# Performance work log

Hardware: AMD Instinct MI355X
Metric: run time of the kernel (lower is better)

The kernel has to match this reference:

```python
import jax, jax.numpy as jnp
import numpy as np

B_SZ = 8
G = 2048
D_MODEL = 512
D_STATE = 128
D_CONV = 4
EXPAND = 2
HEADDIM = 64
D_INNER = EXPAND * D_MODEL          # 1024
NHEADS = D_INNER // HEADDIM         # 16
CONV_DIM = D_INNER + 2 * D_STATE    # 1280
D_IN_PROJ = 2 * D_INNER + 2 * D_STATE + NHEADS  # 2320
ID_DIM = 128
CHR_DIM = 64
N_CHR = 25
F_LOCUS = 32
PATH_DIM = 128
GENE_FEAT = ID_DIM + PATH_DIM + 2 * CHR_DIM  # 384
N_PERT = 10000
P_DIM = 128


def silu(x):
    return x * jax.nn.sigmoid(x)


def causal_dw_conv(x, w, b):
    # x: (B,L,C), w: (C,K), b: (C,)  causal depthwise conv (left pad K-1)
    K = w.shape[1]
    L = x.shape[1]
    xp = jnp.pad(x, ((0, 0), (K - 1, 0), (0, 0)))
    out = b[None, None, :]
    for k in range(K):
        out = out + xp[:, k:k + L, :] * w[:, k][None, None, :]
    return out


def mamba2(u, in_w, conv_w, conv_b, dt_bias, A_log, Dp, norm_w, out_w):
    # u: (B,L,d_model) -> (B,L,d_model); mamba_ssm Mamba2 defaults, ngroups=1
    Bb, L, _ = u.shape
    zxbcdt = u @ in_w.T                                   # (B,L,D_IN_PROJ)
    z = zxbcdt[..., :D_INNER]
    xBC = zxbcdt[..., D_INNER:D_INNER + CONV_DIM]
    dt = zxbcdt[..., D_INNER + CONV_DIM:]                 # (B,L,H)
    xBC = silu(causal_dw_conv(xBC, conv_w, conv_b))
    x = xBC[..., :D_INNER].reshape(Bb, L, NHEADS, HEADDIM)
    Bm = xBC[..., D_INNER:D_INNER + D_STATE]              # (B,L,N)
    Cm = xBC[..., D_INNER + D_STATE:]                     # (B,L,N)
    dt = jax.nn.softplus(dt + dt_bias)                    # (B,L,H)
    dA = jnp.exp(dt * (-jnp.exp(A_log)))                  # (B,L,H)

    def step(h, inp):
        dA_t, dt_t, B_t, C_t, x_t = inp
        h = dA_t[:, :, None, None] * h + jnp.einsum('bh,bn,bhp->bhpn', dt_t, B_t, x_t)
        y = jnp.einsum('bhpn,bn->bhp', h, C_t)
        return h, y

    h0 = jnp.zeros((Bb, NHEADS, HEADDIM, D_STATE), u.dtype)
    xs = (dA.transpose(1, 0, 2), dt.transpose(1, 0, 2),
          Bm.transpose(1, 0, 2), Cm.transpose(1, 0, 2), x.transpose(1, 0, 2, 3))
    _, ys = jax.lax.scan(step, h0, xs)                    # ys: (L,B,H,P)
    y = ys.transpose(1, 0, 2, 3) + Dp[None, None, :, None] * x
    y = y.reshape(Bb, L, D_INNER)
    # gated RMSNorm (norm_before_gate=False): norm(y * silu(z))
    y = y * silu(z)
    y = y * jax.lax.rsqrt(jnp.mean(y * y, axis=-1, keepdims=True) + 1e-5) * norm_w
    return y @ out_w.T


def setup_inputs() -> dict:
    key = jax.random.key(0)
    ks = iter(jax.random.split(key, 48))

    def nrm(shape, scale):
        return jax.random.normal(next(ks), shape, jnp.float32) * scale

    inp = {}
    inp['perturbation_idx'] = jax.random.randint(next(ks), (B_SZ,), 0, N_PERT)
    inp['chr_idx'] = jax.random.randint(next(ks), (G,), 0, N_CHR)
    inp['locus_fourier'] = nrm((G, 2 * F_LOCUS), 1.0)
    inp['pathway_features'] = nrm((G, PATH_DIM), 1.0)
    inp['pert_emb'] = nrm((N_PERT, P_DIM), 0.02)
    inp['gene_id_emb'] = nrm((G, ID_DIM), 0.02)
    inp['chr_emb'] = nrm((N_CHR, CHR_DIM), 0.02)
    inp['locus_w'] = nrm((CHR_DIM, 2 * F_LOCUS), (2 * F_LOCUS) ** -0.5)
    inp['locus_b'] = jnp.zeros((CHR_DIM,), jnp.float32)
    inp['cond_w'] = nrm((GENE_FEAT, P_DIM), P_DIM ** -0.5)
    inp['cond_b'] = jnp.zeros((GENE_FEAT,), jnp.float32)
    inp['in_w'] = nrm((D_MODEL, GENE_FEAT), GENE_FEAT ** -0.5)
    inp['in_b'] = jnp.zeros((D_MODEL,), jnp.float32)
    inp['head_w'] = nrm((1, D_MODEL), D_MODEL ** -0.5)
    inp['head_b'] = jnp.zeros((1,), jnp.float32)
    for p in ('f_', 'b_'):
        inp[p + 'in_w'] = nrm((D_IN_PROJ, D_MODEL), D_MODEL ** -0.5)
        inp[p + 'conv_w'] = nrm((CONV_DIM, D_CONV), D_CONV ** -0.5)
        inp[p + 'conv_b'] = jnp.zeros((CONV_DIM,), jnp.float32)
        inp[p + 'dt_bias'] = nrm((NHEADS,), 0.5)
        inp[p + 'A_log'] = jnp.log(jax.random.uniform(next(ks), (NHEADS,), jnp.float32, 1.0, 16.0))
        inp[p + 'D'] = jnp.ones((NHEADS,), jnp.float32)
        inp[p + 'norm_w'] = jnp.ones((D_INNER,), jnp.float32)
        inp[p + 'out_w'] = nrm((D_MODEL, D_INNER), D_INNER ** -0.5)
    return inp


def reference(perturbation_idx, chr_idx, locus_fourier, pathway_features,
              pert_emb, gene_id_emb, chr_emb, locus_w, locus_b,
              cond_w, cond_b, in_w, in_b, head_w, head_b,
              f_in_w, f_conv_w, f_conv_b, f_dt_bias, f_A_log, f_D, f_norm_w, f_out_w,
              b_in_w, b_conv_w, b_conv_b, b_dt_bias, b_A_log, b_D, b_norm_w, b_out_w):
    B = perturbation_idx.shape[0]
    cond = pert_emb[perturbation_idx] @ cond_w.T + cond_b          # (B, GENE_FEAT)
    e_chr = chr_emb[chr_idx]                                        # (G, CHR_DIM)
    e_locus = jax.nn.gelu(locus_fourier @ locus_w.T + locus_b, approximate=False)
    gene_feat = jnp.concatenate([gene_id_emb, pathway_features, e_chr, e_locus], axis=1)  # (G, GENE_FEAT)
    seq = jnp.concatenate([cond[:, None, :],
                           jnp.broadcast_to(gene_feat[None], (B,) + gene_feat.shape)], axis=1)
    seq = seq @ in_w.T + in_b                                       # (B, G+1, d_model)
    h_fwd = mamba2(seq, f_in_w, f_conv_w, f_conv_b, f_dt_bias, f_A_log, f_D, f_norm_w, f_out_w)
    h_bwd = jnp.flip(mamba2(jnp.flip(seq, axis=1), b_in_w, b_conv_w, b_conv_b,
                            b_dt_bias, b_A_log, b_D, b_norm_w, b_out_w), axis=1)
    H = h_fwd + h_bwd
    return H[:, 1:, :] @ head_w.T + head_b                          # (B, G, 1)
```

## Files before the change

kernel.cpp:

```cpp
#include <hip/hip_runtime.h>
#include <hip/hip_bf16.h>
#include <hip/hip_fp16.h>
#include <math.h>

#define DPROJ 2320
#define CONVD 1280

typedef __attribute__((ext_vector_type(8))) short bf16x8;
typedef __attribute__((ext_vector_type(4))) float f32x4;

__device__ __forceinline__ float siluf(float x) { return x / (1.f + __expf(-x)); }
__device__ __forceinline__ float bfu(unsigned short s) { return __uint_as_float(((unsigned)s) << 16); }
__device__ __forceinline__ unsigned short f2bf(float f) {
    unsigned u = __float_as_uint(f);
    unsigned r = (u + 0x7FFFu + ((u >> 16) & 1u)) >> 16;
    return (unsigned short)r;
}
__device__ __forceinline__ unsigned short f2h(float f) {
    __half h = __float2half(f);
    return *(unsigned short*)&h;
}
__device__ __forceinline__ float h2f(unsigned short s) {
    __half h = *(__half*)&s;
    return __half2float(h);
// ... 165 lines not shown
#pragma unroll
        for (int kk = 0; kk < 16; ++kk) {
            float4 a = *(const float4*)&As[kk][ty * 4];
            float4 w = *(const float4*)&Ws[kk][tx * 4];
            float aa[4] = {a.x, a.y, a.z, a.w}, ww[4] = {w.x, w.y, w.z, w.w};
#pragma unroll
            for (int i = 0; i < 4; ++i)
#pragma unroll
                for (int j = 0; j < 4; ++j) acc[i][j] += aa[i] * ww[j];
        }
    }
#pragma unroll
    for (int i = 0; i < 4; ++i) {
        const int m = bm + ty * 4 + i;
        if (m >= M) continue;
#pragma unroll
        for (int j = 0; j < 4; ++j) {
            const int n = bn + tx * 4 + j;
            if (n >= N) continue;
            float v = acc[i][j] + (bias ? bias[n] : 0.f);
            if (act == 1) v = 0.5f * v * (1.f + erff(v * 0.70710678118654752f));
            C[(size_t)m * ldc + n] = v;
        }
    }
}


__global__ void elem_kernel(const float* __restrict__ zxf, const float* __restrict__ zxb,
                            const float* __restrict__ zxc,
                            const float* __restrict__ fDtB, const float* __restrict__ bDtB,
                            unsigned short* __restrict__ szF, unsigned short* __restrict__ szB,
                            float* __restrict__ dtFsT, float* __restrict__ dtBsT,
                            float* __restrict__ dtFp) {
    size_t idx = (size_t)blockIdx.x * 256 + threadIdx.x;
    const size_t SZ = 2048UL * 1024;
    if (idx < SZ) {
        size_t j = idx >> 10, d = idx & 1023;
        szF[idx] = f2h(siluf(zxf[j * DPROJ + d]));
    } else if (idx < 2 * SZ) {
        size_t k = idx - SZ;
        size_t j = k >> 10, d = k & 1023;
        szB[k] = f2h(siluf(zxb[j * DPROJ + d]));
    } else if (idx < 2 * SZ + 32768) {
        int k = (int)(idx - 2 * SZ);
        int r = k >> 4, hh = k & 15;
        float raw = zxf[(size_t)r * DPROJ + 2304 + hh] + fDtB[hh];
        dtFsT[hh * 2048 + r] = (raw > 20.f) ? raw : log1pf(expf(raw));
    } else if (idx < 2 * SZ + 65536) {
        int k = (int)(idx - 2 * SZ - 32768);
        int r = k >> 4, hh = k & 15;
        float raw = zxb[(size_t)(2047 - r) * DPROJ + 2304 + hh] + bDtB[hh];
        dtBsT[hh * 2048 + r] = (raw > 20.f) ? raw : log1pf(expf(raw));
    } else if (idx < 2 * SZ + 65536 + 128) {
        int k = (int)(idx - 2 * SZ - 65536);
        int b = k >> 4, hh = k & 15;
        float raw = zxc[(size_t)b * DPROJ + 2304 + hh] + fDtB[hh];
        dtFp[k] = (raw > 20.f) ? raw : log1pf(expf(raw));
    }
}

__global__ void cum_kernel(const float* __restrict__ dtFsT, const float* __restrict__ dtBsT,
                           const float* __restrict__ fAlog, const float* __restrict__ bAlog,
                           float* __restrict__ cumF, float* __restrict__ cumB) {
    int id = blockIdx.x * 256 + threadIdx.x;
    int dir = id >> 9, k = id & 511, h = k >> 5, c = k & 31;
    const float* dtT = dir ? dtBsT : dtFsT;
    const float* Al = dir ? bAlog : fAlog;
    float* cum = dir ? cumB : cumF;
    float a = -expf(Al[h]);
    float acc = 0.f;
    for (int s4 = 0; s4 < 16; ++s4) {
        float4 v = *(const float4*)&dtT[h * 2048 + c * 64 + s4 * 4];
        float4 o;
        acc += v.x * a; o.x = acc;
        acc += v.y * a; o.y = acc;
        acc += v.z * a; o.z = acc;
        acc += v.w * a; o.w = acc;
        *(float4*)&cum[h * 2048 + c * 64 + s4 * 4] = o;
    }
}


__global__ void convFsh_kernel(const float* __restrict__ zxf, const float* __restrict__ cw,
                               const float* __restrict__ cb, float* __restrict__ outp,
                               unsigned short* __restrict__ bc16, unsigned short* __restrict__ x16) {
    int idx = blockIdx.x * 256 + threadIdx.x;
    if (idx >= 2045 * 1280) return;
    int t4 = idx / 1280, c = idx % 1280;
    float4 w4 = *(const float4*)&cw[c * 4];
    float acc = cb[c];
    acc += zxf[(size_t)(t4 + 0) * DPROJ + 1024 + c] * w4.x;
    acc += zxf[(size_t)(t4 + 1) * DPROJ + 1024 + c] * w4.y;
    acc += zxf[(size_t)(t4 + 2) * DPROJ + 1024 + c] * w4.z;
    acc += zxf[(size_t)(t4 + 3) * DPROJ + 1024 + c] * w4.w;
    float r = siluf(acc);
    outp[idx] = r;
    if (c >= 1024) bc16[(size_t)t4 * 256 + (c - 1024)] = f2bf(r);
    else           x16[(size_t)t4 * 1024 + c] = f2h(r);
}

__global__ void convFpb_kernel(const float* __restrict__ zxf, const float* __restrict__ zxc,
                               const float* __restrict__ cw, const float* __restrict__ cb,
                               float* __restrict__ outp, unsigned short* __restrict__ bc16,
                               unsigned short* __restrict__ x16) {
    int idx = blockIdx.x * 256 + threadIdx.x;
    int b = idx / 5120;
    int r = idx % 5120;
    int t = r / 1280, c = r % 1280;
    float4 w4 = *(const float4*)&cw[c * 4];
    float w[4] = {w4.x, w4.y, w4.z, w4.w};
    float acc = cb[c];
#pragma unroll
    for (int k = 0; k < 4; ++k) {
        int j = t - 3 + k;
        float x = 0.f;
        if (j == 0)      x = zxc[(size_t)b * DPROJ + 1024 + c];
        else if (j >= 1) x = zxf[(size_t)(j - 1) * DPROJ + 1024 + c];
        acc += x * w[k];
    }
    float rr = siluf(acc);
    outp[idx] = rr;
    if (c >= 1024) bc16[(size_t)(b * 4 + t) * 256 + (c - 1024)] = f2bf(rr);
    else           x16[(size_t)(b * 4 + t) * 1024 + c] = f2h(rr);
}

__global__ void convBsh_kernel(const float* __restrict__ zxb, const float* __restrict__ cw,
                               const float* __restrict__ cb, float* __restrict__ outp,
                               unsigned short* __restrict__ bc16, unsigned short* __restrict__ x16) {
    int idx = blockIdx.x * 256 + threadIdx.x;
    int s = idx / 1280, c = idx % 1280;
    float4 w4 = *(const float4*)&cw[c * 4];
    float w[4] = {w4.x, w4.y, w4.z, w4.w};
    float acc = cb[c];
#pragma unroll
    for (int k = 0; k < 4; ++k) {
        int j = s - 3 + k;
        if (j >= 0) acc += zxb[(size_t)(2047 - j) * DPROJ + 1024 + c] * w[k];
    }
    float r = siluf(acc);
    outp[idx] = r;
    if (c >= 1024) bc16[(size_t)s * 256 + (c - 1024)] = f2bf(r);
    else           x16[(size_t)s * 1024 + c] = f2h(r);
}


__global__ __launch_bounds__(256) void intra_kernel(
    const unsigned short* __restrict__ bcF, const unsigned short* __restrict__ bcFp,
    const unsigned short* __restrict__ bcB,
    const float* __restrict__ convFs, const float* __restrict__ convFp,
    const float* __restrict__ convBs,
    const float* __restrict__ dtFsT, const float* __restrict__ dtBsT,
    const float* __restrict__ cumF, const float* __restrict__ cumB,
    unsigned short* __restrict__ YiF0, unsigned short* __restrict__ YiFs,
    unsigned short* __restrict__ YiB,
    unsigned short* __restrict__ UF0, unsigned short* __restrict__ UFs,
    unsigned short* __restrict__ UB) {
    __shared__ __align__(16) unsigned char smraw[63232];
    unsigned short* Bt = (unsigned short*)smraw;
    unsigned short* Ct = (unsigned short*)(smraw + 17408);
    unsigned short* Sm = (unsigned short*)(smraw + 17408);
    unsigned short* BT = (unsigned short*)(smraw + 34816);
    unsigned short* XT = (unsigned short*)(smraw + 53248);
    float* scum = (float*)(smraw + 62464);
    float* sdt  = scum + 64;
    float* se   = scum + 128;

    const int iid = blockIdx.x;
    int dir, b = 0, h, c;
    unsigned short *Yout, *Uout;
    if (iid < 128)      { dir = 0; b = iid >> 4; h = iid & 15; c = 0;
                          Yout = YiF0 + (size_t)(b * 16 + h) * 4096; Uout = UF0 + (size_t)(b * 16 + h) * 8192; }
    else if (iid < 624) { int k = iid - 128; dir = 0; c = 1 + (k >> 4); h = k & 15;
                          Yout = YiFs + (size_t)(c * 16 + h) * 4096; Uout = UFs + (size_t)(c * 16 + h) * 8192; }
    else                { int k = iid - 624; dir = 1; c = k >> 4; h = k & 15;
                          Yout = YiB + (size_t)(c * 16 + h) * 4096;  Uout = UB + (size_t)(c * 16 + h) * 8192; }
    const float* dtAT = dir ? dtBsT : dtFsT;
    const float* cumA = dir ? cumB : cumF;

    const int tid = threadIdx.x;
    const int lane = tid & 63, wave = tid >> 6;
    const int quad = lane >> 4, l15 = lane & 15;

    {
        int r = tid >> 2, q = tid & 3;
        const unsigned short* bsrc;
        const float* xrow;
        if (dir == 0) {
            int t = 64 * c + 1 + r;
            if (t < 4) { bsrc = bcFp + (size_t)(b * 4 + t) * 256; xrow = convFp + (size_t)(b * 4 + t) * CONVD; }
            else       { bsrc = bcF + (size_t)(t - 4) * 256;      xrow = convFs + (size_t)(t - 4) * CONVD; }
        } else {
            int s = 64 * c + r;
            bsrc = bcB + (size_t)s * 256;
            xrow = convBs + (size_t)s * CONVD;
        }
#pragma unroll
        for (int i = 0; i < 4; ++i) {
            int n0 = q * 32 + i * 8;
            uint4 v = *(const uint4*)&bsrc[n0];
            *(uint4*)&Bt[r * 136 + n0] = v;
            const unsigned short* pv = (const unsigned short*)&v;
#pragma unroll
            for (int jj = 0; jj < 8; ++jj) BT[(n0 + jj) * 72 + r] = pv[jj];
        }
#pragma unroll
        for (int i = 0; i < 4; ++i) {
            int n0 = q * 32 + i * 8;
            uint4 v = *(const uint4*)&bsrc[128 + n0];
            *(uint4*)&Ct[r * 136 + n0] = v;
        }
#pragma unroll
        for (int i = 0; i < 4; ++i) {
            int p0 = (q + 4 * i) * 4;
            float4 v = *(const float4*)&xrow[h * 64 + p0];
            XT[(p0 + 0) * 72 + r] = f2bf(v.x);
            XT[(p0 + 1) * 72 + r] = f2bf(v.y);
            XT[(p0 + 2) * 72 + r] = f2bf(v.z);
            XT[(p0 + 3) * 72 + r] = f2bf(v.w);
        }
        if (tid < 64) {
            int j = 64 * c + tid;
            scum[tid] = cumA[h * 2048 + j];
            sdt[tid] = dtAT[h * 2048 + j];
        }
    }
    __syncthreads();
    if (tid < 64) se[tid] = __expf(scum[63] - scum[tid]) * sdt[tid];

    const int tm = (wave >> 1) * 32, sn = (wave & 1) * 32;
    f32x4 acc1[2][2];
#pragma unroll
    for (int i = 0; i < 2; ++i)
#pragma unroll
        for (int j = 0; j < 2; ++j) acc1[i][j] = (f32x4){0.f, 0.f, 0.f, 0.f};
#pragma unroll
    for (int ks = 0; ks < 4; ++ks) {
        bf16x8 af[2], bfr[2];
#pragma unroll
        for (int i = 0; i < 2; ++i)
            af[i] = *(const bf16x8*)&Ct[(tm + i * 16 + l15) * 136 + ks * 32 + quad * 8];
#pragma unroll
        for (int j = 0; j < 2; ++j)
            bfr[j] = *(const bf16x8*)&Bt[(sn + j * 16 + l15) * 136 + ks * 32 + quad * 8];
#pragma unroll
        for (int i = 0; i < 2; ++i)
#pragma unroll
            for (int j = 0; j < 2; ++j)
                acc1[i][j] = __builtin_amdgcn_mfma_f32_16x16x32_bf16(af[i], bfr[j], acc1[i][j], 0, 0, 0);
    }
    __syncthreads();

#pragma unroll
    for (int j = 0; j < 2; ++j) {
        int s = sn + j * 16 + l15;
        float cs = scum[s], ds = sdt[s];
#pragma unroll
        for (int i = 0; i < 2; ++i) {
#pragma unroll
            for (int r = 0; r < 4; ++r) {
                int t = tm + i * 16 + quad * 4 + r;
                float v = (s <= t) ? __expf(scum[t] - cs) * ds * acc1[i][j][r] : 0.f;
                Sm[t * 72 + s] = f2bf(v);
            }
        }
    }
    __syncthreads();

    const int pm = (wave >> 1) * 32, tn = (wave & 1) * 32;
    f32x4 acc2[2][2];
#pragma unroll
    for (int i = 0; i < 2; ++i)
#pragma unroll
        for (int j = 0; j < 2; ++j) acc2[i][j] = (f32x4){0.f, 0.f, 0.f, 0.f};
#pragma unroll
    for (int ks = 0; ks < 2; ++ks) {
        bf16x8 af[2], bfr[2];
#pragma unroll
        for (int i = 0; i < 2; ++i)
            af[i] = *(const bf16x8*)&XT[(pm + i * 16 + l15) * 72 + ks * 32 + quad * 8];
#pragma unroll
        for (int j = 0; j < 2; ++j)
            bfr[j] = *(const bf16x8*)&Sm[(tn + j * 16 + l15) * 72 + ks * 32 + quad * 8];
#pragma unroll
        for (int i = 0; i < 2; ++i)
#pragma unroll
            for (int j = 0; j < 2; ++j)
                acc2[i][j] = __builtin_amdgcn_mfma_f32_16x16x32_bf16(af[i], bfr[j], acc2[i][j], 0, 0, 0);
    }
#pragma unroll
    for (int i = 0; i < 2; ++i)
#pragma unroll
        for (int j = 0; j < 2; ++j) {
            int t = tn + j * 16 + l15;
            int p0 = pm + i * 16 + quad * 4;
            ushort4 o = make_ushort4(f2bf(acc2[i][j][0]), f2bf(acc2[i][j][1]),
                                     f2bf(acc2[i][j][2]), f2bf(acc2[i][j][3]));
            *(ushort4*)&Yout[t * 64 + p0] = o;
        }

    const int nm = wave * 32;
    f32x4 acc3[2][4];
#pragma unroll
    for (int i = 0; i < 2; ++i)
#pragma unroll
        for (int j = 0; j < 4; ++j) acc3[i][j] = (f32x4){0.f, 0.f, 0.f, 0.f};
#pragma unroll
    for (int ks = 0; ks < 2; ++ks) {
        float ev[8];
#pragma unroll
        for (int jj = 0; jj < 8; ++jj) ev[jj] = se[ks * 32 + quad * 8 + jj];
        bf16x8 bfx[4];
#pragma unroll
        for (int j = 0; j < 4; ++j) {
            bf16x8 xs = *(const bf16x8*)&XT[(j * 16 + l15) * 72 + ks * 32 + quad * 8];
#pragma unroll
            for (int jj = 0; jj < 8; ++jj)
                bfx[j][jj] = (short)f2bf(bfu((unsigned short)xs[jj]) * ev[jj]);
        }
        bf16x8 af[2];
#pragma unroll
        for (int i = 0; i < 2; ++i)
            af[i] = *(const bf16x8*)&BT[(nm + i * 16 + l15) * 72 + ks * 32 + quad * 8];
#pragma unroll
        for (int i = 0; i < 2; ++i)
#pragma unroll
            for (int j = 0; j < 4; ++j)
                acc3[i][j] = __builtin_amdgcn_mfma_f32_16x16x32_bf16(af[i], bfx[j], acc3[i][j], 0, 0, 0);
    }
#pragma unroll
    for (int i = 0; i < 2; ++i)
#pragma unroll
        for (int j = 0; j < 4; ++j) {
            int p = j * 16 + l15;
            int n0 = nm + i * 16 + quad * 4;
            ushort4 o = make_ushort4(f2bf(acc3[i][j][0]), f2bf(acc3[i][j][1]),
                                     f2bf(acc3[i][j][2]), f2bf(acc3[i][j][3]));
            *(ushort4*)&Uout[p * 128 + n0] = o;
        }
}


__global__ void cbm_kernel(const float* __restrict__ convFs, const float* __restrict__ convFp,
                           const float* __restrict__ dtFp, const float* __restrict__ cumF,
                           const unsigned short* __restrict__ UF0,
                           float* __restrict__ cb0, unsigned short* __restrict__ Mb) {
    int blk = blockIdx.x, tid = threadIdx.x;
    if (blk < 32) {
        int idx = blk * 256 + tid;
        int b = idx >> 10, r = idx & 1023, h = r >> 6, tl = r & 63;
        int t = tl + 1;
        const float* crow = (t < 4) ? convFp + (size_t)(b * 4 + t) * CONVD : convFs + (size_t)(t - 4) * CONVD;
        const float* b0 = convFp + (size_t)(b * 4) * CONVD;
        float s = 0.f;
        for (int n = 0; n < 128; ++n) s += crow[1152 + n] * b0[1024 + n];
        cb0[(b * 16 + h) * 64 + tl] = s * dtFp[b * 16 + h];
    } else {
        int bh = blk - 32;
        int b = bh >> 4, h = bh & 15;
        float D0 = __expf(cumF[h * 2048 + 63]);
        float dt0 = dtFp[b * 16 + h];
        const float* row0 = convFp + (size_t)(b * 4) * CONVD;
        const unsigned short* u = UF0 + (size_t)(b * 16 + h) * 8192;
        unsigned short* m = Mb + (size_t)(b * 16 + h) * 8192;
        for (int e4 = tid; e4 < 2048; e4 += 256) {
            int e = e4 * 4, p = e >> 7, n0 = e & 127;
            float s = D0 * dt0 * row0[h * 64 + p];
            float4 B4 = *(const float4*)&row0[1024 + n0];
            ushort4 uv = *(const ushort4*)&u[e];
            ushort4 o = make_ushort4(f2bf(s * B4.x + bfu(uv.x)), f2bf(s * B4.y + bfu(uv.y)),
                                     f2bf(s * B4.z + bfu(uv.z)), f2bf(s * B4.w + bfu(uv.w)));
            *(ushort4*)&m[e] = o;
        }
    }
}


__global__ void tpsi_kernel(const unsigned short* __restrict__ UFs, const unsigned short* __restrict__ UB,
                            const float* __restrict__ cumF, const float* __restrict__ cumB,
                            unsigned short* __restrict__ Tst, float* __restrict__ psiF) {
    int blk = blockIdx.x;
    int dir = blk >> 7, h = (blk >> 3) & 15, q8 = blk & 7;
    int tid = threadIdx.x;
    const unsigned short* U = dir ? UB : UFs;
    const float* cum = dir ? cumB : cumF;
    unsigned short* T = Tst + (size_t)(dir * 16 + h) * 32 * 8192;
    if (dir == 0 && q8 == 0 && tid == 0) {
        float ps = 1.f;
        for (int c = 1; c < 32; ++c) {
            psiF[h * 32 + c] = ps;
            ps *= __expf(cumF[h * 2048 + c * 64 + 63]);
        }
    }
    const size_t e = (size_t)q8 * 1024 + 4 * tid;
    float4 st = make_float4(0.f, 0.f, 0.f, 0.f);
    const int c0 = dir ? 0 : 1;
    ushort4 u = *(const ushort4*)&U[((size_t)c0 * 16 + h) * 8192 + e];
    for (int c = c0; c < 32; ++c) {
        ushort4 un = make_ushort4(0, 0, 0, 0);
        if (c + 1 < 32) un = *(const ushort4*)&U[((size_t)(c + 1) * 16 + h) * 8192 + e];
        float Dc = __expf(cum[h * 2048 + c * 64 + 63]);
        ushort4 o = make_ushort4(f2bf(st.x), f2bf(st.y), f2bf(st.z), f2bf(st.w));
        *(ushort4*)&T[(size_t)c * 8192 + e] = o;
        st.x = Dc * st.x + bfu(u.x);
        st.y = Dc * st.y + bfu(u.y);
        st.z = Dc * st.z + bfu(u.z);
        st.w = Dc * st.w + bfu(u.w);
        u = un;
    }
}


__global__ __launch_bounds__(256) void yt_kernel(
    const unsigned short* __restrict__ bcF, const unsigned short* __restrict__ bcB,
    const unsigned short* __restrict__ Tst,
    unsigned short* __restrict__ YtF, unsigned short* __restrict__ YtB) {
    const int iid = blockIdx.x;
    int dir, h, c;
    if (iid < 496) { dir = 0; c = 1 + (iid >> 4); h = iid & 15; }
    else           { int k = iid - 496; dir = 1; c = k >> 4; h = k & 15; }
    const unsigned short* Cbase = (dir == 0)
        ? bcF + ((size_t)(64 * c - 3)) * 256 + 128
        : bcB + ((size_t)(64 * c)) * 256 + 128;
    const unsigned short* Tp = Tst + ((size_t)(dir * 16 + h) * 32 + c) * 8192;
    unsigned short* Yt = (dir == 0 ? YtF : YtB) + (size_t)(c * 16 + h) * 4096;
    const int tid = threadIdx.x;
    const int lane = tid & 63, wave = tid >> 6;
    const int quad = lane >> 4, l15 = lane & 15;
    const int pm = (wave >> 1) * 32, tb = (wave & 1) * 32;
    f32x4 acc[2][2];
#pragma unroll
    for (int i = 0; i < 2; ++i)
#pragma unroll
        for (int j = 0; j < 2; ++j) acc[i][j] = (f32x4){0.f, 0.f, 0.f, 0.f};
#pragma unroll
    for (int ks = 0; ks < 4; ++ks) {
        bf16x8 af[2], bfr[2];
#pragma unroll
        for (int i = 0; i < 2; ++i)
            af[i] = *(const bf16x8*)&Tp[(size_t)(pm + i * 16 + l15) * 128 + ks * 32 + quad * 8];
#pragma unroll
        for (int j = 0; j < 2; ++j)
            bfr[j] = *(const bf16x8*)&Cbase[(size_t)(tb + j * 16 + l15) * 256 + ks * 32 + quad * 8];
#pragma unroll
        for (int i = 0; i < 2; ++i)
#pragma unroll
            for (int j = 0; j < 2; ++j)
                acc[i][j] = __builtin_amdgcn_mfma_f32_16x16x32_bf16(af[i], bfr[j], acc[i][j], 0, 0, 0);
    }
#pragma unroll
    for (int i = 0; i < 2; ++i)
#pragma unroll
        for (int j = 0; j < 2; ++j) {
            int t = tb + j * 16 + l15;
            int p0 = pm + i * 16 + quad * 4;
            ushort4 o = make_ushort4(f2bf(acc[i][j][0]), f2bf(acc[i][j][1]),
                                     f2bf(acc[i][j][2]), f2bf(acc[i][j][3]));
            *(ushort4*)&Yt[t * 64 + p0] = o;
        }
}


__global__ __launch_bounds__(256, 4) void gate_kernel(
    const unsigned short* __restrict__ bcF,
    const unsigned short* __restrict__ Mb, const float* __restrict__ psiF,
    const unsigned short* __restrict__ YtF, const unsigned short* __restrict__ YtB,
    const unsigned short* __restrict__ xF16, const unsigned short* __restrict__ xFp16,
    const unsigned short* __restrict__ xB16,
    const unsigned short* __restrict__ szF, const unsigned short* __restrict__ szB,
    const float* __restrict__ convFp,
    const float* __restrict__ cumF, const float* __restrict__ cumB,
    const unsigned short* __restrict__ YiF0, const unsigned short* __restrict__ YiFs,
    const unsigned short* __restrict__ YiB,
    const float* __restrict__ cb0,
    const float* __restrict__ fD, const float* __restrict__ bD,
    const float* __restrict__ wf2, const float* __restrict__ wb2,
    float* __restrict__ aF, float* __restrict__ aB) {
    __shared__ __align__(16) float Ysm[64 * 68];

    const int iid = blockIdx.x;
    int dir, b = 0, h, c;
    if (iid < 4096) { dir = 0; b = iid >> 9; int r = iid & 511; h = r >> 5; c = r & 31; }
    else            { int k = iid - 4096; dir = 1; h = k >> 5; c = k & 31; }
    const int tid = threadIdx.x, tx = tid & 15, ty = tid >> 4;
    const int lane = tid & 63, wave = tid >> 6;
    const int quad = lane >> 4, l15 = lane & 15;
    const bool fwdG = (dir == 0 && c > 0);

    if (fwdG) {
        const unsigned short* Cbase = bcF + ((size_t)(64 * c - 3)) * 256 + 128;
        const unsigned short* Mp = Mb + (size_t)(b * 16 + h) * 8192;
        const int pm = (wave >> 1) * 32, tb = (wave & 1) * 32;
        f32x4 acc[2][2];
#pragma unroll
        for (int i = 0; i < 2; ++i)
#pragma unroll
            for (int j = 0; j < 2; ++j) acc[i][j] = (f32x4){0.f, 0.f, 0.f, 0.f};
#pragma unroll
        for (int ks = 0; ks < 4; ++ks) {
            bf16x8 af[2], bfr[2];
#pragma unroll
            for (int i = 0; i < 2; ++i)
                af[i] = *(const bf16x8*)&Mp[(size_t)(pm + i * 16 + l15) * 128 + ks * 32 + quad * 8];
#pragma unroll
            for (int j = 0; j < 2; ++j)
                bfr[j] = *(const bf16x8*)&Cbase[(size_t)(tb + j * 16 + l15) * 256 + ks * 32 + quad * 8];
#pragma unroll
            for (int i = 0; i < 2; ++i)
#pragma unroll
                for (int j = 0; j < 2; ++j)
                    acc[i][j] = __builtin_amdgcn_mfma_f32_16x16x32_bf16(af[i], bfr[j], acc[i][j], 0, 0, 0);
        }
#pragma unroll
        for (int i = 0; i < 2; ++i)
#pragma unroll
            for (int j = 0; j < 2; ++j)
                *(f32x4*)&Ysm[(tb + j * 16 + l15) * 68 + pm + i * 16 + quad * 4] = acc[i][j];
        __syncthreads();
    }

    const float Dh = (dir ? bD : fD)[h];
    const float* wvp = dir ? wb2 : wf2;
    float4 wreg = *(const float4*)&wvp[h * 64 + tx * 4];
    const float* cumA = dir ? cumB : cumF;
    const float psi = fwdG ? psiF[h * 32 + c] : 0.f;
    const unsigned short* Ytp = fwdG ? (YtF + (size_t)(c * 16 + h) * 4096)
                                     : (dir ? (YtB + (size_t)(c * 16 + h) * 4096) : nullptr);
    float4 x0v = make_float4(0.f, 0.f, 0.f, 0.f);
    float cbv[4] = {0.f, 0.f, 0.f, 0.f};
    if (dir == 0 && c == 0) {
        x0v = *(const float4*)&convFp[(size_t)(b * 4) * CONVD + h * 64 + tx * 4];
#pragma unroll
        for (int i = 0; i < 4; ++i) cbv[i] = cb0[(b * 16 + h) * 64 + (ty + 16 * i)];
    }

    float rawet[4];
    ushort4 yi4a[4], x4a[4], z4a[4], yt4a[4];
    float4 cm4a[4];
#pragma unroll
    for (int i = 0; i < 4; ++i) {
        int tl = ty + 16 * i;
        int j = 64 * c + tl;
        rawet[i] = cumA[h * 2048 + j];
        const unsigned short *Yi, *xp, *zp;
        if (dir == 0) {
            Yi = (c == 0) ? YiF0 + (size_t)(b * 16 + h) * 4096 : YiFs + (size_t)(c * 16 + h) * 4096;
            if (c == 0) {
                int t = j + 1;
                xp = (t < 4) ? xFp16 + (size_t)(b * 4 + t) * 1024 : xF16 + (size_t)(t - 4) * 1024;
            } else {
                xp = xF16 + (size_t)(64 * c + tl - 3) * 1024;
            }
            zp = szF + (size_t)j * 1024;
        } else {
            Yi = YiB + (size_t)(c * 16 + h) * 4096;
            xp = xB16 + (size_t)j * 1024;
            zp = szB + (size_t)(2047 - j) * 1024;
        }
        yi4a[i] = *(const ushort4*)&Yi[tl * 64 + tx * 4];
        x4a[i] = *(const ushort4*)&xp[h * 64 + tx * 4];
        z4a[i] = *(const ushort4*)&zp[h * 64 + tx * 4];
        yt4a[i] = Ytp ? *(const ushort4*)&Ytp[tl * 64 + tx * 4] : make_ushort4(0, 0, 0, 0);
        cm4a[i] = fwdG ? *(const float4*)&Ysm[tl * 68 + tx * 4] : make_float4(0.f, 0.f, 0.f, 0.f);
    }

#pragma unroll
    for (int i = 0; i < 4; ++i) {
        int j = 64 * c + ty + 16 * i;
        float et = __expf(rawet[i]);
        float yv[4] = {bfu(yi4a[i].x), bfu(yi4a[i].y), bfu(yi4a[i].z), bfu(yi4a[i].w)};
        float xa[4] = {h2f(x4a[i].x), h2f(x4a[i].y), h2f(x4a[i].z), h2f(x4a[i].w)};
        float sza[4] = {h2f(z4a[i].x), h2f(z4a[i].y), h2f(z4a[i].z), h2f(z4a[i].w)};
        float ya[4] = {bfu(yt4a[i].x) + psi * cm4a[i].x, bfu(yt4a[i].y) + psi * cm4a[i].y,
                       bfu(yt4a[i].z) + psi * cm4a[i].z, bfu(yt4a[i].w) + psi * cm4a[i].w};
        float x0a[4] = {x0v.x, x0v.y, x0v.z, x0v.w};
        float wa[4] = {wreg.x, wreg.y, wreg.z, wreg.w};
        float a1 = 0.f, a2 = 0.f;
#pragma unroll
        for (int w = 0; w < 4; ++w) {
            float tot = yv[w] + et * (ya[w] + cbv[i] * x0a[w]) + Dh * xa[w];
            float g = tot * sza[w];
            a1 += g * wa[w];
            a2 += g * g;
        }
#pragma unroll
        for (int m = 1; m < 16; m <<= 1) {
            a1 += __shfl_xor(a1, m);
            a2 += __shfl_xor(a2, m);
        }
        if (tx == 0) {
            if (dir == 0) {
                size_t o = ((size_t)(b * 2048 + j) * 16 + h) * 2;
                aF[o] = a1; aF[o + 1] = a2;
            } else {
                int g = 2047 - j;
                size_t o = ((size_t)g * 16 + h) * 2;
                aB[o] = a1; aB[o + 1] = a2;
            }
        }
    }
}


__global__ void final_kernel(const float* __restrict__ aF, const float* __restrict__ aB,
                             const float* __restrict__ headB, float* __restrict__ out) {
    int idx = blockIdx.x * 256 + threadIdx.x;
    int b = idx >> 11, g = idx & 2047;
    const float* pf = aF + ((size_t)(b * 2048 + g)) * 32;
    const float* pb = aB + (size_t)g * 32;
    float f1 = 0.f, f2 = 0.f, b1 = 0.f, b2 = 0.f;
#pragma unroll
    for (int h = 0; h < 16; ++h) {
        f1 += pf[2 * h]; f2 += pf[2 * h + 1];
        b1 += pb[2 * h]; b2 += pb[2 * h + 1];
    }
    out[idx] = f1 * rsqrtf(f2 * (1.f / 1024.f) + 1e-5f) +
               b1 * rsqrtf(b2 * (1.f / 1024.f) + 1e-5f) + headB[0];
}


extern "C" void kernel_launch(void* const* d_in, const int* in_sizes, int n_in,
                              void* d_out, int out_size, void* d_ws, size_t ws_size,
                              hipStream_t stream) {
    const int*   pidx   = (const int*)  d_in[0];
    const int*   chridx = (const int*)  d_in[1];
    const float* locusF = (const float*)d_in[2];
    const float* pathF  = (const float*)d_in[3];
    const float* pertE  = (const float*)d_in[4];
    const float* gidE   = (const float*)d_in[5];
    const float* chrE   = (const float*)d_in[6];
    const float* locusW = (const float*)d_in[7];
    const float* locusB = (const float*)d_in[8];
    const float* condW  = (const float*)d_in[9];
    const float* condB  = (const float*)d_in[10];
    const float* inW    = (const float*)d_in[11];
    const float* inB    = (const float*)d_in[12];
    const float* headW  = (const float*)d_in[13];
    const float* headB  = (const float*)d_in[14];
    const float* fInW   = (const float*)d_in[15];
    const float* fCw    = (const float*)d_in[16];
    const float* fCb    = (const float*)d_in[17];
    const float* fDtB   = (const float*)d_in[18];
    const float* fAlog  = (const float*)d_in[19];
    const float* fDp    = (const float*)d_in[20];
    const float* fNw    = (const float*)d_in[21];
    const float* fOutW  = (const float*)d_in[22];
    const float* bInW   = (const float*)d_in[23];
    const float* bCw    = (const float*)d_in[24];
    const float* bCb    = (const float*)d_in[25];
    const float* bDtB   = (const float*)d_in[26];
    const float* bAlog  = (const float*)d_in[27];
    const float* bDp    = (const float*)d_in[28];
    const float* bNw    = (const float*)d_in[29];
    const float* bOutW  = (const float*)d_in[30];
    float* out = (float*)d_out;
    (void)in_sizes; (void)n_in; (void)out_size; (void)ws_size;

    char* base = (char*)d_ws;
    size_t off = 0;
    auto allocf = [&](size_t n) -> float* {
        char* r = base + off; off += ((n * 4 + 63) & ~(size_t)63); return (float*)r; };
    auto allocu = [&](size_t n) -> unsigned short* {
        char* r = base + off; off += ((n * 2 + 63) & ~(size_t)63); return (unsigned short*)r; };

    float* gf     = allocf(2048UL * 384);
    float* cond   = allocf(8UL * 384);
    float* cemb   = allocf(8UL * 128);
    float* ug     = allocf(2048UL * 512);
    float* uc     = allocf(8UL * 512);
    float* zxf    = allocf(2048UL * DPROJ);
    float* zxb    = allocf(2048UL * DPROJ);
    float* zxc    = allocf(8UL * DPROJ);
    float* convFs = allocf(2045UL * CONVD);
    float* convFp = allocf(8UL * 4 * CONVD);
    float* convBs = allocf(2048UL * CONVD);
    float* dtFsT  = allocf(16UL * 2048);
    float* dtFp   = allocf(128);
    float* dtBsT  = allocf(16UL * 2048);
    float* cumF   = allocf(16UL * 2048);
    float* cumB   = allocf(16UL * 2048);
    float* wf2    = allocf(1024);
    float* wb2    = allocf(1024);
    float* cb0    = allocf(8UL * 16 * 64);
    float* psiF   = allocf(16UL * 32);
    float* aF     = allocf(8UL * 2048 * 16 * 2);
    float* aB     = allocf(2048UL * 16 * 2);
    unsigned short* YiF0 = allocu(8UL * 16 * 4096);
    unsigned short* YiFs = allocu(32UL * 16 * 4096);
    unsigned short* YiB  = allocu(32UL * 16 * 4096);
    unsigned short* UF0  = allocu(8UL * 16 * 8192);
    unsigned short* UFs  = allocu(32UL * 16 * 8192);
    unsigned short* UB   = allocu(32UL * 16 * 8192);
    unsigned short* Mb   = allocu(8UL * 16 * 8192);
    unsigned short* Tst  = allocu(2UL * 16 * 32 * 8192);
    unsigned short* bcF  = allocu(2045UL * 256);
    unsigned short* bcFp = allocu(32UL * 256);
    unsigned short* bcB  = allocu(2048UL * 256);
    unsigned short* YtF  = allocu(32UL * 16 * 4096);
    unsigned short* YtB  = allocu(32UL * 16 * 4096);
    unsigned short* xF16 = allocu(2045UL * 1024);
    unsigned short* xFp16= allocu(32UL * 1024);
    unsigned short* xB16 = allocu(2048UL * 1024);
    unsigned short* szF  = allocu(2048UL * 1024);
    unsigned short* szB  = allocu(2048UL * 1024);
    unsigned short* gf2   = allocu(2048UL * 384);
    unsigned short* inW2  = allocu(512UL * 384);
    unsigned short* ug2   = allocu(2048UL * 512);
    unsigned short* fInW2 = allocu(2432UL * 512);
    unsigned short* bInW2 = allocu(2432UL * 512);

    gg_kernel<<<3077, 256, 0, stream>>>(chridx, gidE, pathF, chrE, pidx, pertE, gf, cemb, wf2, wb2);
    wfold_kernel<<<128, 256, 0, stream>>>(headW, fOutW, fNw, bOutW, bNw, wf2, wb2);
    gemm_kernel<<<dim3(1, 32), 256, 0, stream>>>(locusF, locusW, locusB, gf + 320, 2048, 64, 64, 384, 1);
    gemm_kernel<<<dim3(6, 1), 256, 0, stream>>>(cemb, condW, condB, cond, 8, 384, 128, 384, 0);

    tobf4_kernel<<<13568, 256, 0, stream>>>(inW, fInW, bInW, gf, inW2, fInW2, bInW2, gf2);

    mfma_gemm_kernel<<<dim3(4, 16), 256, 0, stream>>>(gf2, inW2, inB, ug, 512, 384, 512);
    gemm_kernel<<<dim3(8, 1), 256, 0, stream>>>(cond, inW, inB, uc, 8, 512, 384, 512, 0);

    tobf_kernel<<<(2048 * 512 + 255) / 256, 256, 0, stream>>>(ug, ug2, 2048, 512, 2048);
    mfma_gemm_kernel<<<dim3(19, 16), 256, 0, stream>>>(ug2, fInW2, nullptr, zxf, 2320, 512, 2320);
    mfma_gemm_kernel<<<dim3(19, 16), 256, 0, stream>>>(ug2, bInW2, nullptr, zxb, 2320, 512, 2320);
    gemm_kernel<<<dim3(37, 1), 256, 0, stream>>>(uc, fInW, nullptr, zxc, 8, DPROJ, 512, DPROJ, 0);

    elem_kernel<<<16641, 256, 0, stream>>>(zxf, zxb, zxc, fDtB, bDtB, szF, szB, dtFsT, dtBsT, dtFp);
    cum_kernel<<<4, 256, 0, stream>>>(dtFsT, dtBsT, fAlog, bAlog, cumF, cumB);
    convFsh_kernel<<<(2045 * 1280 + 255) / 256, 256, 0, stream>>>(zxf, fCw, fCb, convFs, bcF, xF16);
    convFpb_kernel<<<160, 256, 0, stream>>>(zxf, zxc, fCw, fCb, convFp, bcFp, xFp16);
    convBsh_kernel<<<10240, 256, 0, stream>>>(zxb, bCw, bCb, convBs, bcB, xB16);
    intra_kernel<<<1136, 256, 0, stream>>>(bcF, bcFp, bcB, convFs, convFp, convBs,
                                           dtFsT, dtBsT, cumF, cumB,
                                           YiF0, YiFs, YiB, UF0, UFs, UB);
    cbm_kernel<<<160, 256, 0, stream>>>(convFs, convFp, dtFp, cumF, UF0, cb0, Mb);
    tpsi_kernel<<<256, 256, 0, stream>>>(UFs, UB, cumF, cumB, Tst, psiF);
    yt_kernel<<<1008, 256, 0, stream>>>(bcF, bcB, Tst, YtF, YtB);
    gate_kernel<<<4608, 256, 0, stream>>>(bcF, Mb, psiF, YtF, YtB, xF16, xFp16, xB16,
                                          szF, szB, convFp, cumF, cumB,
                                          YiF0, YiFs, YiB, cb0, fDp, bDp, wf2, wb2, aF, aB);
    final_kernel<<<64, 256, 0, stream>>>(aF, aB, headB, out);
}
```

Measured before the change: 401.3 us.

## Drop fp32 conv outputs, feed bf16 x to intra, batch gate chunks per block

```diff
diff --git a/kernel.cpp b/kernel.cpp
--- a/kernel.cpp
+++ b/kernel.cpp
@@ -271,7 +271,7 @@
 
 
 __global__ void convFsh_kernel(const float* __restrict__ zxf, const float* __restrict__ cw,
-                               const float* __restrict__ cb, float* __restrict__ outp,
+                               const float* __restrict__ cb,
                                unsigned short* __restrict__ bc16, unsigned short* __restrict__ x16) {
     int idx = blockIdx.x * 256 + threadIdx.x;
     if (idx >= 2045 * 1280) return;
@@ -283,9 +283,8 @@
     acc += zxf[(size_t)(t4 + 2) * DPROJ + 1024 + c] * w4.z;
     acc += zxf[(size_t)(t4 + 3) * DPROJ + 1024 + c] * w4.w;
     float r = siluf(acc);
-    outp[idx] = r;
     if (c >= 1024) bc16[(size_t)t4 * 256 + (c - 1024)] = f2bf(r);
-    else           x16[(size_t)t4 * 1024 + c] = f2h(r);
+    else           x16[(size_t)t4 * 1024 + c] = f2bf(r);
 }
 
 __global__ void convFpb_kernel(const float* __restrict__ zxf, const float* __restrict__ zxc,
@@ -310,11 +309,11 @@
     float rr = siluf(acc);
     outp[idx] = rr;
     if (c >= 1024) bc16[(size_t)(b * 4 + t) * 256 + (c - 1024)] = f2bf(rr);
-    else           x16[(size_t)(b * 4 + t) * 1024 + c] = f2h(rr);
+    else           x16[(size_t)(b * 4 + t) * 1024 + c] = f2bf(rr);
 }
 
 __global__ void convBsh_kernel(const float* __restrict__ zxb, const float* __restrict__ cw,
-                               const float* __restrict__ cb, float* __restrict__ outp,
+                               const float* __restrict__ cb,
                                unsigned short* __restrict__ bc16, unsigned short* __restrict__ x16) {
     int idx = blockIdx.x * 256 + threadIdx.x;
     int s = idx / 1280, c = idx % 1280;
@@ -327,17 +326,16 @@
         if (j >= 0) acc += zxb[(size_t)(2047 - j) * DPROJ + 1024 + c] * w[k];
     }
     float r = siluf(acc);
-    outp[idx] = r;
     if (c >= 1024) bc16[(size_t)s * 256 + (c - 1024)] = f2bf(r);
-    else           x16[(size_t)s * 1024 + c] = f2h(r);
+    else           x16[(size_t)s * 1024 + c] = f2bf(r);
 }
 
 
 __global__ __launch_bounds__(256) void intra_kernel(
     const unsigned short* __restrict__ bcF, const unsigned short* __restrict__ bcFp,
     const unsigned short* __restrict__ bcB,
-    const float* __restrict__ convFs, const float* __restrict__ convFp,
-    const float* __restrict__ convBs,
+    const unsigned short* __restrict__ xF16, const unsigned short* __restrict__ xFp16,
+    const unsigned short* __restrict__ xB16,
     const float* __restrict__ dtFsT, const float* __restrict__ dtBsT,
     const float* __restrict__ cumF, const float* __restrict__ cumB,
     unsigned short* __restrict__ YiF0, unsigned short* __restrict__ YiFs,
@@ -372,16 +370,15 @@
 
     {
         int r = tid >> 2, q = tid & 3;
-        const unsigned short* bsrc;
-        const float* xrow;
+        const unsigned short *bsrc, *xsrc;
         if (dir == 0) {
             int t = 64 * c + 1 + r;
-            if (t < 4) { bsrc = bcFp + (size_t)(b * 4 + t) * 256; xrow = convFp + (size_t)(b * 4 + t) * CONVD; }
-            else       { bsrc = bcF + (size_t)(t - 4) * 256;      xrow = convFs + (size_t)(t - 4) * CONVD; }
+            if (t < 4) { bsrc = bcFp + (size_t)(b * 4 + t) * 256; xsrc = xFp16 + (size_t)(b * 4 + t) * 1024; }
+            else       { bsrc = bcF + (size_t)(t - 4) * 256;      xsrc = xF16 + (size_t)(t - 4) * 1024; }
         } else {
             int s = 64 * c + r;
             bsrc = bcB + (size_t)s * 256;
-            xrow = convBs + (size_t)s * CONVD;
+            xsrc = xB16 + (size_t)s * 1024;
         }
 #pragma unroll
         for (int i = 0; i < 4; ++i) {
@@ -399,13 +396,11 @@
             *(uint4*)&Ct[r * 136 + n0] = v;
         }
 #pragma unroll
-        for (int i = 0; i < 4; ++i) {
-            int p0 = (q + 4 * i) * 4;
-            float4 v = *(const float4*)&xrow[h * 64 + p0];
-            XT[(p0 + 0) * 72 + r] = f2bf(v.x);
-            XT[(p0 + 1) * 72 + r] = f2bf(v.y);
-            XT[(p0 + 2) * 72 + r] = f2bf(v.z);
-            XT[(p0 + 3) * 72 + r] = f2bf(v.w);
+        for (int k = 0; k < 2; ++k) {
+            uint4 v = *(const uint4*)&xsrc[h * 64 + q * 16 + k * 8];
+            const unsigned short* pv = (const unsigned short*)&v;
+#pragma unroll
+            for (int jj = 0; jj < 8; ++jj) XT[(q * 16 + k * 8 + jj) * 72 + r] = pv[jj];
         }
         if (tid < 64) {
             int j = 64 * c + tid;
@@ -529,7 +524,7 @@
 }
 
 
-__global__ void cbm_kernel(const float* __restrict__ convFs, const float* __restrict__ convFp,
+__global__ void cbm_kernel(const float* __restrict__ convFp, const unsigned short* __restrict__ bcF,
                            const float* __restrict__ dtFp, const float* __restrict__ cumF,
                            const unsigned short* __restrict__ UF0,
                            float* __restrict__ cb0, unsigned short* __restrict__ Mb) {
@@ -538,10 +533,15 @@
         int idx = blk * 256 + tid;
         int b = idx >> 10, r = idx & 1023, h = r >> 6, tl = r & 63;
         int t = tl + 1;
-        const float* crow = (t < 4) ? convFp + (size_t)(b * 4 + t) * CONVD : convFs + (size_t)(t - 4) * CONVD;
         const float* b0 = convFp + (size_t)(b * 4) * CONVD;
         float s = 0.f;
-        for (int n = 0; n < 128; ++n) s += crow[1152 + n] * b0[1024 + n];
+        if (t < 4) {
+            const float* crow = convFp + (size_t)(b * 4 + t) * CONVD;
+            for (int n = 0; n < 128; ++n) s += crow[1152 + n] * b0[1024 + n];
+        } else {
+            const unsigned short* cr = bcF + (size_t)(t - 4) * 256 + 128;
+            for (int n = 0; n < 128; ++n) s += bfu(cr[n]) * b0[1024 + n];
+        }
         cb0[(b * 16 + h) * 64 + tl] = s * dtFp[b * 16 + h];
     } else {
         int bh = blk - 32;
@@ -649,7 +649,7 @@
 }
 
 
-__global__ __launch_bounds__(256, 4) void gate_kernel(
+__global__ __launch_bounds__(256) void gate_kernel(
     const unsigned short* __restrict__ bcF,
     const unsigned short* __restrict__ Mb, const float* __restrict__ psiF,
     const unsigned short* __restrict__ YtF, const unsigned short* __restrict__ YtB,
@@ -667,123 +667,134 @@
     __shared__ __align__(16) float Ysm[64 * 68];
 
     const int iid = blockIdx.x;
-    int dir, b = 0, h, c;
-    if (iid < 4096) { dir = 0; b = iid >> 9; int r = iid & 511; h = r >> 5; c = r & 31; }
-    else            { int k = iid - 4096; dir = 1; h = k >> 5; c = k & 31; }
+    int dir, b = 0, h, cg;
+    if (iid < 1024) { dir = 0; b = iid >> 7; int r = iid & 127; h = r >> 3; cg = r & 7; }
+    else            { int k = iid - 1024; dir = 1; h = k >> 3; cg = k & 7; }
     const int tid = threadIdx.x, tx = tid & 15, ty = tid >> 4;
     const int lane = tid & 63, wave = tid >> 6;
     const int quad = lane >> 4, l15 = lane & 15;
-    const bool fwdG = (dir == 0 && c > 0);
-
-    if (fwdG) {
-        const unsigned short* Cbase = bcF + ((size_t)(64 * c - 3)) * 256 + 128;
-        const unsigned short* Mp = Mb + (size_t)(b * 16 + h) * 8192;
-        const int pm = (wave >> 1) * 32, tb = (wave & 1) * 32;
-        f32x4 acc[2][2];
-#pragma unroll
-        for (int i = 0; i < 2; ++i)
-#pragma unroll
-            for (int j = 0; j < 2; ++j) acc[i][j] = (f32x4){0.f, 0.f, 0.f, 0.f};
-#pragma unroll
-        for (int ks = 0; ks < 4; ++ks) {
-            bf16x8 af[2], bfr[2];
-#pragma unroll
-            for (int i = 0; i < 2; ++i)
-                af[i] = *(const bf16x8*)&Mp[(size_t)(pm + i * 16 + l15) * 128 + ks * 32 + quad * 8];
-#pragma unroll
-            for (int j = 0; j < 2; ++j)
-                bfr[j] = *(const bf16x8*)&Cbase[(size_t)(tb + j * 16 + l15) * 256 + ks * 32 + quad * 8];
-#pragma unroll
-            for (int i = 0; i < 2; ++i)
-#pragma unroll
-                for (int j = 0; j < 2; ++j)
-                    acc[i][j] = __builtin_amdgcn_mfma_f32_16x16x32_bf16(af[i], bfr[j], acc[i][j], 0, 0, 0);
-        }
-#pragma unroll
-        for (int i = 0; i < 2; ++i)
-#pragma unroll
-            for (int j = 0; j < 2; ++j)
-                *(f32x4*)&Ysm[(tb + j * 16 + l15) * 68 + pm + i * 16 + quad * 4] = acc[i][j];
-        __syncthreads();
-    }
 
     const float Dh = (dir ? bD : fD)[h];
     const float* wvp = dir ? wb2 : wf2;
     float4 wreg = *(const float4*)&wvp[h * 64 + tx * 4];
     const float* cumA = dir ? cumB : cumF;
-    const float psi = fwdG ? psiF[h * 32 + c] : 0.f;
-    const unsigned short* Ytp = fwdG ? (YtF + (size_t)(c * 16 + h) * 4096)
-                                     : (dir ? (YtB + (size_t)(c * 16 + h) * 4096) : nullptr);
-    float4 x0v = make_float4(0.f, 0.f, 0.f, 0.f);
-    float cbv[4] = {0.f, 0.f, 0.f, 0.f};
-    if (dir == 0 && c == 0) {
-        x0v = *(const float4*)&convFp[(size_t)(b * 4) * CONVD + h * 64 + tx * 4];
-#pragma unroll
-        for (int i = 0; i < 4; ++i) cbv[i] = cb0[(b * 16 + h) * 64 + (ty + 16 * i)];
-    }
-
-    float rawet[4];
-    ushort4 yi4a[4], x4a[4], z4a[4], yt4a[4];
-    float4 cm4a[4];
-#pragma unroll
-    for (int i = 0; i < 4; ++i) {
-        int tl = ty + 16 * i;
-        int j = 64 * c + tl;
-        rawet[i] = cumA[h * 2048 + j];
-        const unsigned short *Yi, *xp, *zp;
-        if (dir == 0) {
-            Yi = (c == 0) ? YiF0 + (size_t)(b * 16 + h) * 4096 : YiFs + (size_t)(c * 16 + h) * 4096;
-            if (c == 0) {
-                int t = j + 1;
-                xp = (t < 4) ? xFp16 + (size_t)(b * 4 + t) * 1024 : xF16 + (size_t)(t - 4) * 1024;
+
+    const int pm = (wave >> 1) * 32, tb = (wave & 1) * 32;
+    bf16x8 mfr[4][2];
+    if (dir == 0) {
+        const unsigned short* Mp = Mb + (size_t)(b * 16 + h) * 8192;
+#pragma unroll
+        for (int ks = 0; ks < 4; ++ks)
+#pragma unroll
+            for (int i = 0; i < 2; ++i)
+                mfr[ks][i] = *(const bf16x8*)&Mp[(size_t)(pm + i * 16 + l15) * 128 + ks * 32 + quad * 8];
+    }
+
+    for (int cc = 0; cc < 4; ++cc) {
+        const int c = cg * 4 + cc;
+        const bool fwdG = (dir == 0 && c > 0);
+        if (fwdG) {
+            if (cc > 0) __syncthreads();
+            const unsigned short* Cbase = bcF + ((size_t)(64 * c - 3)) * 256 + 128;
+            f32x4 acc[2][2];
+#pragma unroll
+            for (int i = 0; i < 2; ++i)
+#pragma unroll
+                for (int j = 0; j < 2; ++j) acc[i][j] = (f32x4){0.f, 0.f, 0.f, 0.f};
+#pragma unroll
+            for (int ks = 0; ks < 4; ++ks) {
+                bf16x8 bfr[2];
+#pragma unroll
+                for (int j = 0; j < 2; ++j)
+                    bfr[j] = *(const bf16x8*)&Cbase[(size_t)(tb + j * 16 + l15) * 256 + ks * 32 + quad * 8];
+#pragma unroll
+                for (int i = 0; i < 2; ++i)
+#pragma unroll
+                    for (int j = 0; j < 2; ++j)
+                        acc[i][j] = __builtin_amdgcn_mfma_f32_16x16x32_bf16(mfr[ks][i], bfr[j], acc[i][j], 0, 0, 0);
+            }
+#pragma unroll
+            for (int i = 0; i < 2; ++i)
+#pragma unroll
+                for (int j = 0; j < 2; ++j)
+                    *(f32x4*)&Ysm[(tb + j * 16 + l15) * 68 + pm + i * 16 + quad * 4] = acc[i][j];
+            __syncthreads();
+        }
+
+        const float psi = fwdG ? psiF[h * 32 + c] : 0.f;
+        const unsigned short* Ytp = fwdG ? (YtF + (size_t)(c * 16 + h) * 4096)
+                                         : (dir ? (YtB + (size_t)(c * 16 + h) * 4096) : nullptr);
+        float4 x0v = make_float4(0.f, 0.f, 0.f, 0.f);
+        float cbv[4] = {0.f, 0.f, 0.f, 0.f};
+        if (dir == 0 && c == 0) {
+            x0v = *(const float4*)&convFp[(size_t)(b * 4) * CONVD + h * 64 + tx * 4];
+#pragma unroll
+            for (int i = 0; i < 4; ++i) cbv[i] = cb0[(b * 16 + h) * 64 + (ty + 16 * i)];
+        }
+
+        float rawet[4];
+        ushort4 yi4a[4], x4a[4], z4a[4], yt4a[4];
+        float4 cm4a[4];
+#pragma unroll
+        for (int i = 0; i < 4; ++i) {
+            int tl = ty + 16 * i;
+            int j = 64 * c + tl;
+            rawet[i] = cumA[h * 2048 + j];
+            const unsigned short *Yi, *xp, *zp;
+            if (dir == 0) {
+                Yi = (c == 0) ? YiF0 + (size_t)(b * 16 + h) * 4096 : YiFs + (size_t)(c * 16 + h) * 4096;
+                if (c == 0) {
+                    int t = j + 1;
+                    xp = (t < 4) ? xFp16 + (size_t)(b * 4 + t) * 1024 : xF16 + (size_t)(t - 4) * 1024;
+                } else {
+                    xp = xF16 + (size_t)(64 * c + tl - 3) * 1024;
+                }
+                zp = szF + (size_t)j * 1024;
             } else {
-                xp = xF16 + (size_t)(64 * c + tl - 3) * 1024;
+                Yi = YiB + (size_t)(c * 16 + h) * 4096;
+                xp = xB16 + (size_t)j * 1024;
+                zp = szB + (size_t)(2047 - j) * 1024;
             }
-            zp = szF + (size_t)j * 1024;
-        } else {
-            Yi = YiB + (size_t)(c * 16 + h) * 4096;
-            xp = xB16 + (size_t)j * 1024;
-            zp = szB + (size_t)(2047 - j) * 1024;
-        }
-        yi4a[i] = *(const ushort4*)&Yi[tl * 64 + tx * 4];
-        x4a[i] = *(const ushort4*)&xp[h * 64 + tx * 4];
-        z4a[i] = *(const ushort4*)&zp[h * 64 + tx * 4];
-        yt4a[i] = Ytp ? *(const ushort4*)&Ytp[tl * 64 + tx * 4] : make_ushort4(0, 0, 0, 0);
-        cm4a[i] = fwdG ? *(const float4*)&Ysm[tl * 68 + tx * 4] : make_float4(0.f, 0.f, 0.f, 0.f);
-    }
-
-#pragma unroll
-    for (int i = 0; i < 4; ++i) {
-        int j = 64 * c + ty + 16 * i;
-        float et = __expf(rawet[i]);
-        float yv[4] = {bfu(yi4a[i].x), bfu(yi4a[i].y), bfu(yi4a[i].z), bfu(yi4a[i].w)};
-        float xa[4] = {h2f(x4a[i].x), h2f(x4a[i].y), h2f(x4a[i].z), h2f(x4a[i].w)};
-        float sza[4] = {h2f(z4a[i].x), h2f(z4a[i].y), h2f(z4a[i].z), h2f(z4a[i].w)};
-        float ya[4] = {bfu(yt4a[i].x) + psi * cm4a[i].x, bfu(yt4a[i].y) + psi * cm4a[i].y,
-                       bfu(yt4a[i].z) + psi * cm4a[i].z, bfu(yt4a[i].w) + psi * cm4a[i].w};
-        float x0a[4] = {x0v.x, x0v.y, x0v.z, x0v.w};
-        float wa[4] = {wreg.x, wreg.y, wreg.z, wreg.w};
-        float a1 = 0.f, a2 = 0.f;
-#pragma unroll
-        for (int w = 0; w < 4; ++w) {
-            float tot = yv[w] + et * (ya[w] + cbv[i] * x0a[w]) + Dh * xa[w];
-            float g = tot * sza[w];
-            a1 += g * wa[w];
-            a2 += g * g;
-        }
-#pragma unroll
-        for (int m = 1; m < 16; m <<= 1) {
-            a1 += __shfl_xor(a1, m);
-            a2 += __shfl_xor(a2, m);
-        }
-        if (tx == 0) {
-            if (dir == 0) {
-                size_t o = ((size_t)(b * 2048 + j) * 16 + h) * 2;
-                aF[o] = a1; aF[o + 1] = a2;
-            } else {
-                int g = 2047 - j;
-                size_t o = ((size_t)g * 16 + h) * 2;
-                aB[o] = a1; aB[o + 1] = a2;
+            yi4a[i] = *(const ushort4*)&Yi[tl * 64 + tx * 4];
+            x4a[i] = *(const ushort4*)&xp[h * 64 + tx * 4];
+            z4a[i] = *(const ushort4*)&zp[h * 64 + tx * 4];
+            yt4a[i] = Ytp ? *(const ushort4*)&Ytp[tl * 64 + tx * 4] : make_ushort4(0, 0, 0, 0);
+            cm4a[i] = fwdG ? *(const float4*)&Ysm[tl * 68 + tx * 4] : make_float4(0.f, 0.f, 0.f, 0.f);
+        }
+
+#pragma unroll
+        for (int i = 0; i < 4; ++i) {
+            int j = 64 * c + ty + 16 * i;
+            float et = __expf(rawet[i]);
+            float yv[4] = {bfu(yi4a[i].x), bfu(yi4a[i].y), bfu(yi4a[i].z), bfu(yi4a[i].w)};
+            float xa[4] = {bfu(x4a[i].x), bfu(x4a[i].y), bfu(x4a[i].z), bfu(x4a[i].w)};
+            float sza[4] = {h2f(z4a[i].x), h2f(z4a[i].y), h2f(z4a[i].z), h2f(z4a[i].w)};
+            float ya[4] = {bfu(yt4a[i].x) + psi * cm4a[i].x, bfu(yt4a[i].y) + psi * cm4a[i].y,
+                           bfu(yt4a[i].z) + psi * cm4a[i].z, bfu(yt4a[i].w) + psi * cm4a[i].w};
+            float x0a[4] = {x0v.x, x0v.y, x0v.z, x0v.w};
+            float wa[4] = {wreg.x, wreg.y, wreg.z, wreg.w};
+            float a1 = 0.f, a2 = 0.f;
+#pragma unroll
+            for (int w = 0; w < 4; ++w) {
+                float tot = yv[w] + et * (ya[w] + cbv[i] * x0a[w]) + Dh * xa[w];
+                float g = tot * sza[w];
+                a1 += g * wa[w];
+                a2 += g * g;
+            }
+#pragma unroll
+            for (int m = 1; m < 16; m <<= 1) {
+                a1 += __shfl_xor(a1, m);
+                a2 += __shfl_xor(a2, m);
+            }
+            if (tx == 0) {
+                if (dir == 0) {
+                    size_t o = ((size_t)(b * 2048 + j) * 16 + h) * 2;
+                    aF[o] = a1; aF[o + 1] = a2;
+                } else {
+                    int g = 2047 - j;
+                    size_t o = ((size_t)g * 16 + h) * 2;
+                    aB[o] = a1; aB[o + 1] = a2;
+                }
             }
         }
     }
@@ -859,9 +870,7 @@
     float* zxf    = allocf(2048UL * DPROJ);
     float* zxb    = allocf(2048UL * DPROJ);
     float* zxc    = allocf(8UL * DPROJ);
-    float* convFs = allocf(2045UL * CONVD);
     float* convFp = allocf(8UL * 4 * CONVD);
-    float* convBs = allocf(2048UL * CONVD);
     float* dtFsT  = allocf(16UL * 2048);
     float* dtFp   = allocf(128);
     float* dtBsT  = allocf(16UL * 2048);
@@ -914,16 +923,16 @@
 
     elem_kernel<<<16641, 256, 0, stream>>>(zxf, zxb, zxc, fDtB, bDtB, szF, szB, dtFsT, dtBsT, dtFp);
     cum_kernel<<<4, 256, 0, stream>>>(dtFsT, dtBsT, fAlog, bAlog, cumF, cumB);
-    convFsh_kernel<<<(2045 * 1280 + 255) / 256, 256, 0, stream>>>(zxf, fCw, fCb, convFs, bcF, xF16);
+    convFsh_kernel<<<(2045 * 1280 + 255) / 256, 256, 0, stream>>>(zxf, fCw, fCb, bcF, xF16);
     convFpb_kernel<<<160, 256, 0, stream>>>(zxf, zxc, fCw, fCb, convFp, bcFp, xFp16);
-    convBsh_kernel<<<10240, 256, 0, stream>>>(zxb, bCw, bCb, convBs, bcB, xB16);
-    intra_kernel<<<1136, 256, 0, stream>>>(bcF, bcFp, bcB, convFs, convFp, convBs,
+    convBsh_kernel<<<10240, 256, 0, stream>>>(zxb, bCw, bCb, bcB, xB16);
+    intra_kernel<<<1136, 256, 0, stream>>>(bcF, bcFp, bcB, xF16, xFp16, xB16,
                                            dtFsT, dtBsT, cumF, cumB,
                                            YiF0, YiFs, YiB, UF0, UFs, UB);
-    cbm_kernel<<<160, 256, 0, stream>>>(convFs, convFp, dtFp, cumF, UF0, cb0, Mb);
+    cbm_kernel<<<160, 256, 0, stream>>>(convFp, bcF, dtFp, cumF, UF0, cb0, Mb);
     tpsi_kernel<<<256, 256, 0, stream>>>(UFs, UB, cumF, cumB, Tst, psiF);
     yt_kernel<<<1008, 256, 0, stream>>>(bcF, bcB, Tst, YtF, YtB);
-    gate_kernel<<<4608, 256, 0, stream>>>(bcF, Mb, psiF, YtF, YtB, xF16, xFp16, xB16,
+    gate_kernel<<<1152, 256, 0, stream>>>(bcF, Mb, psiF, YtF, YtB, xF16, xFp16, xB16,
                                           szF, szB, convFp, cumF, cumB,
                                           YiF0, YiFs, YiB, cb0, fDp, bDp, wf2, wb2, aF, aB);
     final_kernel<<<64, 256, 0, stream>>>(aF, aB, headB, out);
```

Result: no change. 398.4 us (-0.7%).
